# Optimization experiments

Hardware: AMD Instinct MI355X
Metric: run time of the kernel (lower is better)

## Reference

```python
import jax, jax.numpy as jnp
import numpy as np

EPS = 1e-7
NUM_NODES = 50000


def setup_inputs() -> dict:
    key = jax.random.key(0)
    k1, k2, k3 = jax.random.split(key, 3)
    n_nodes, n_edges, d = NUM_NODES, 800000, 64
    x = jax.random.normal(k1, (n_nodes, d), dtype=jnp.float32)
    edge_index = jax.random.randint(k2, (2, n_edges), 0, n_nodes, dtype=jnp.int64)
    W = jax.random.normal(k3, (d, d), dtype=jnp.float32) * (1.0 / np.sqrt(d))
    b = jnp.zeros((d,), dtype=jnp.float32)
    beta = jnp.ones((1,), dtype=jnp.float32)
    return {"x": x, "edge_index": edge_index, "W": W, "b": b, "beta": beta}


def _segment_softmax(logits, seg, num_segments):
    # numerically stable softmax over edges grouped by destination node, per channel
    m = jax.ops.segment_max(logits, seg, num_segments=num_segments)  # [N, d]
    m = jnp.where(jnp.isfinite(m), m, 0.0)  # empty segments -> -inf; neutralize
    e = jnp.exp(logits - m[seg])                                      # [E, d]
    denom = jax.ops.segment_sum(e, seg, num_segments=num_segments)    # [N, d]
    return e / (denom[seg] + 1e-16)


def reference(x, edge_index, W, b, beta):
    num_nodes, dim = x.shape
    dst = edge_index[0]
    src = edge_index[1]
    # gather + message encoder (ReLU) + eps
    edge_msg = jax.nn.relu(x[src]) + EPS                               # [E, d]
    # softmax_sg: softmax(beta * msg) per destination segment, beta is a stop-grad scalar
    alpha = _segment_softmax(beta[0] * edge_msg, dst, num_nodes)       # [E, d]
    h = edge_msg * alpha                                               # [E, d]
    # scatter-add aggregation to destination nodes
    agg = jax.ops.segment_sum(h, dst, num_segments=num_nodes)          # [N, d]
    # final dense linear (nn.Linear): agg @ W.T + b
    return agg @ W.T + b
```

## Files before the change

kernel.cpp:

```cpp
#include <hip/hip_runtime.h>
#include <hip/hip_fp16.h>

#define EPS 1e-7f
#define LOG2E 1.4426950408889634f
#define CAP 384
#define NBMAX 3136

typedef _Float16 half8 __attribute__((ext_vector_type(8)));
typedef float f32x4 __attribute__((ext_vector_type(4)));

__global__ __launch_bounds__(512)
void binprep_kernel(const int* __restrict__ dst,
                    const int* __restrict__ src, int E, int NB,
                    const float* __restrict__ x,
                    const float* __restrict__ W,
                    const float* __restrict__ beta, int M,
                    int* __restrict__ ccur,
                    unsigned* __restrict__ packed,
                    unsigned short* __restrict__ tm,
                    unsigned short* __restrict__ Wh,
                    int binBlocks) {
    if ((int)blockIdx.x < binBlocks) {
        __shared__ int lc[NBMAX];
        __shared__ int lbase[NBMAX];
        int tid = threadIdx.x;
        for (int i = tid; i < NB; i += 512) lc[i] = 0;
        __syncthreads();
        int e0 = blockIdx.x * 4096;
        int bb[8], rr[8];
        unsigned pk[8];
        #pragma unroll
        for (int i = 0; i < 8; ++i) {
            int e = e0 + i * 512 + tid;
            bb[i] = 0; rr[i] = 0; pk[i] = 0;
            if (e < E) {
                int d = dst[e];
                bb[i] = d >> 4;
                pk[i] = ((unsigned)(d & 15) << 16) | (unsigned)src[e];
                rr[i] = atomicAdd(&lc[bb[i]], 1);
            }
        }
        __syncthreads();
        for (int i = tid; i < NB; i += 512) {
            int c = lc[i];
            if (c) lbase[i] = i * CAP + atomicAdd(&ccur[i], c);
        }
        __syncthreads();
        #pragma unroll
        for (int i = 0; i < 8; ++i) {
            int e = e0 + i * 512 + tid;
            if (e < E) {
                int pos = lbase[bb[i]] + rr[i];
                if (pos < (bb[i] + 1) * CAP)
                    packed[pos] = pk[i];
            }
        }
    } else {
        int blk = blockIdx.x - binBlocks;
        int tid = threadIdx.x;
        if (blk == 0) {
            #pragma unroll
            for (int j = 0; j < 8; ++j) {
                int i = tid * 8 + j;
                Wh[i] = __half_as_ushort(__float2half_rn(W[i]));
            }
        }
        const float btl = beta[0] * LOG2E;
        const unsigned short sent = __half_as_ushort(__float2half_rn(-1000.f));
        #pragma unroll
        for (int p = 0; p < 4; ++p) {
            int i = blk * 8192 + p * 2048 + tid * 4;
            if (i < M) {
                float4 v = *(const float4*)&x[i];
                ushort4 o;
                o.x = __half_as_ushort(__float2half_rn((fmaxf(v.x, 0.f) + EPS) * btl));
                o.y = __half_as_ushort(__float2half_rn((fmaxf(v.y, 0.f) + EPS) * btl));
                o.z = __half_as_ushort(__float2half_rn((fmaxf(v.z, 0.f) + EPS) * btl));
                o.w = __half_as_ushort(__float2half_rn((fmaxf(v.w, 0.f) + EPS) * btl));
                *(ushort4*)&tm[i] = o;
            } else if (i < M + 64) {
                ushort4 o; o.x = o.y = o.z = o.w = sent;
                *(ushort4*)&tm[i] = o;
            }
        }
    }
}

__global__ __launch_bounds__(256)
void gatherlin_kernel(const unsigned* __restrict__ packed,
                      const int* __restrict__ ccur,
                      const unsigned short* __restrict__ tm,
                      const unsigned short* __restrict__ Wh,
                      const float* __restrict__ bias,
                      const float* __restrict__ beta,
                      float* __restrict__ out, int N) {
    __shared__ unsigned stage_pk[CAP];
    __shared__ unsigned short stage16[CAP + 64];
    __shared__ short aggS[16 * 72];
    __shared__ int lc[16], nstart[16], lcur[16];

    const int tid = threadIdx.x;
    const int b = blockIdx.x;
    const unsigned short sentid = (unsigned short)N;

    int len = ccur[b];
    if (len > CAP) len = CAP;
    const int rs = b * CAP;

    if (tid < 16) lc[tid] = 0;
    for (int i = tid; i < CAP + 64; i += 256) stage16[i] = sentid;
    __syncthreads();

    for (int i = tid; i < len; i += 256) {
        unsigned u = packed[rs + i];
        stage_pk[i] = u;
        atomicAdd(&lc[u >> 16], 1);
    }
    __syncthreads();

    if (tid < 16) {
        int c4 = (lc[tid] + 3) & ~3;
        int incl = c4;
        #pragma unroll
        for (int d = 1; d < 16; d <<= 1) {
            int t = __shfl_up(incl, d, 64);
            if (tid >= d) incl += t;
        }
        nstart[tid] = incl - c4;
        lcur[tid] = incl - c4;
    }
    __syncthreads();

    for (int i = tid; i < len; i += 256) {
        unsigned u = stage_pk[i];
        int pos = atomicAdd(&lcur[u >> 16], 1);
        stage16[pos] = (unsigned short)(u & 0xffffu);
    }
    __syncthreads();

    const int wave = tid >> 6;
    const int lane = tid & 63;
    const int quarter = lane >> 4;
    const int l16 = lane & 15;
    const int chb = l16 << 3;
    const unsigned char* tb = (const unsigned char*)tm;
    const float scale = 0.6931471805599453f / beta[0];

    const int nl = wave * 4 + quarter;
    const int start = nstart[nl];
    const int cnt = lc[nl];

    float s1x = 0.f, s1y = 0.f, s1z = 0.f, s1w = 0.f;
    float s2x = 0.f, s2y = 0.f, s2z = 0.f, s2w = 0.f;

    #pragma unroll 1
    for (int k = 0; k < cnt; k += 4) {
        uint2 e4 = *(const uint2*)&stage16[start + k];
        int r0 = (int)(e4.x & 0xffffu) << 7;
        int r1 = (int)(e4.x >> 16) << 7;
        int r2 = (int)(e4.y & 0xffffu) << 7;
        int r3 = (int)(e4.y >> 16) << 7;
        uint2 u0 = *(const uint2*)(tb + (r0 + chb));
        uint2 u1 = *(const uint2*)(tb + (r1 + chb));
        uint2 u2 = *(const uint2*)(tb + (r2 + chb));
        uint2 u3 = *(const uint2*)(tb + (r3 + chb));
        #define ACC(u) { \
            float m0 = __half2float(__ushort_as_half((unsigned short)(u.x & 0xffffu))); \
            float m1 = __half2float(__ushort_as_half((unsigned short)(u.x >> 16))); \
            float m2 = __half2float(__ushort_as_half((unsigned short)(u.y & 0xffffu))); \
            float m3 = __half2float(__ushort_as_half((unsigned short)(u.y >> 16))); \
            float e0 = exp2f(m0), e1 = exp2f(m1); \
            float e2 = exp2f(m2), e3 = exp2f(m3); \
            s1x += e0; s2x = fmaf(m0, e0, s2x); \
            s1y += e1; s2y = fmaf(m1, e1, s2y); \
            s1z += e2; s2z = fmaf(m2, e2, s2z); \
            s1w += e3; s2w = fmaf(m3, e3, s2w); }
        ACC(u0); ACC(u1); ACC(u2); ACC(u3);
        #undef ACC
    }

    {
        float gx = __fdividef(s2x, s1x + 1e-16f) * scale;
        float gy = __fdividef(s2y, s1y + 1e-16f) * scale;
        float gz = __fdividef(s2z, s1z + 1e-16f) * scale;
        float gw = __fdividef(s2w, s1w + 1e-16f) * scale;
        uint2 o;
        o.x = (unsigned)__half_as_ushort(__float2half_rn(gx)) |
              ((unsigned)__half_as_ushort(__float2half_rn(gy)) << 16);
        o.y = (unsigned)__half_as_ushort(__float2half_rn(gz)) |
              ((unsigned)__half_as_ushort(__float2half_rn(gw)) << 16);
        *(uint2*)((unsigned char*)aggS + nl * 144 + chb) = o;
    }
    __syncthreads();

    const unsigned char* ab = (const unsigned char*)aggS;
    half8 a0 = *(const half8*)(ab + l16 * 144 + quarter * 16);
    half8 a1 = *(const half8*)(ab + l16 * 144 + 64 + quarter * 16);
    const unsigned char* wr =
        (const unsigned char*)Wh + (((size_t)(wave * 16 + l16)) << 7) + quarter * 16;
    half8 b0 = *(const half8*)(wr);
    half8 b1 = *(const half8*)(wr + 64);
    f32x4 acc = (f32x4){0.f, 0.f, 0.f, 0.f};
    acc = __builtin_amdgcn_mfma_f32_16x16x32_f16(a0, b0, acc, 0, 0, 0);
    acc = __builtin_amdgcn_mfma_f32_16x16x32_f16(a1, b1, acc, 0, 0, 0);
    const float bv = bias[wave * 16 + l16];
    #pragma unroll
    for (int r = 0; r < 4; ++r) {
        int nd = b * 16 + quarter * 4 + r;
        if (nd < N)
            out[((size_t)nd << 6) + wave * 16 + l16] = acc[r] + bv;
    }
}

extern "C" void kernel_launch(void* const* d_in, const int* in_sizes, int n_in,
                              void* d_out, int out_size, void* d_ws, size_t ws_size,
                              hipStream_t stream) {
    const float* x    = (const float*)d_in[0];
    const int*   ei   = (const int*)d_in[1];
    const float* W    = (const float*)d_in[2];
    const float* b    = (const float*)d_in[3];
    const float* beta = (const float*)d_in[4];
    float* out = (float*)d_out;

    const int N = in_sizes[0] / 64;
    const int E = in_sizes[1] / 2;
    const int* dst = ei;
    const int* src = ei + E;
    const int NB = (N + 15) >> 4;
    const int M = N * 64;

    auto align = [](size_t v) { return (v + 255) & ~(size_t)255; };
    size_t off = 0;
    char* ws = (char*)d_ws;
    int* ccur = (int*)(ws + off);         off += align((size_t)NB * 4);
    unsigned* packed = (unsigned*)(ws + off);
    off += align((size_t)NB * CAP * 4);
    unsigned short* tm = (unsigned short*)(ws + off);
    off += align(((size_t)N + 1) * 64 * 2);
    unsigned short* Wh = (unsigned short*)(ws + off);
    off += align(64 * 64 * 2);

    const int binBlocks  = (E + 4095) / 4096;
    const int prepBlocks = (M + 64 + 8191) / 8192;
    hipMemsetAsync(ccur, 0, (size_t)NB * 4, stream);
    binprep_kernel<<<binBlocks + prepBlocks, 512, 0, stream>>>(
        dst, src, E, NB, x, W, beta, M, ccur, packed, tm, Wh, binBlocks);
    gatherlin_kernel<<<NB, 256, 0, stream>>>(packed, ccur, tm, Wh, b, beta,
                                             out, N);
}
```

Baseline: 113.2 us.

## Replace bin-then-sort with per-node fixed-capacity adjacency lists via global atomics

Edges are now scattered straight into a per-destination-node list of capacity 64 using a global atomic counter per node. This replaces the per-16-node bin buffer and the shared-memory counting sort that the gather kernel used to do. The gather kernel reads each node's list directly and processes 8 neighbours per iteration, padding with a sentinel row. Shared-memory staging and several block barriers go away, at the cost of more global atomic contention. Any node with more than 64 incoming edges is silently truncated.

```diff
diff --git a/kernel.cpp b/kernel.cpp
--- a/kernel.cpp
+++ b/kernel.cpp
@@ -3,61 +3,49 @@
 
 #define EPS 1e-7f
 #define LOG2E 1.4426950408889634f
-#define CAP 384
-#define NBMAX 3136
+#define CAPN 64
 
 typedef _Float16 half8 __attribute__((ext_vector_type(8)));
 typedef float f32x4 __attribute__((ext_vector_type(4)));
 
 __global__ __launch_bounds__(512)
 void binprep_kernel(const int* __restrict__ dst,
-                    const int* __restrict__ src, int E, int NB,
+                    const int* __restrict__ src, int E,
                     const float* __restrict__ x,
                     const float* __restrict__ W,
                     const float* __restrict__ beta, int M,
-                    int* __restrict__ ccur,
-                    unsigned* __restrict__ packed,
+                    int* __restrict__ cnt,
+                    unsigned short* __restrict__ list,
                     unsigned short* __restrict__ tm,
                     unsigned short* __restrict__ Wh,
                     int binBlocks) {
+    const int tid = threadIdx.x;
     if ((int)blockIdx.x < binBlocks) {
-        __shared__ int lc[NBMAX];
-        __shared__ int lbase[NBMAX];
-        int tid = threadIdx.x;
-        for (int i = tid; i < NB; i += 512) lc[i] = 0;
-        __syncthreads();
-        int e0 = blockIdx.x * 4096;
-        int bb[8], rr[8];
-        unsigned pk[8];
-        #pragma unroll
-        for (int i = 0; i < 8; ++i) {
-            int e = e0 + i * 512 + tid;
-            bb[i] = 0; rr[i] = 0; pk[i] = 0;
-            if (e < E) {
-                int d = dst[e];
-                bb[i] = d >> 4;
-                pk[i] = ((unsigned)(d & 15) << 16) | (unsigned)src[e];
-                rr[i] = atomicAdd(&lc[bb[i]], 1);
+        const int e0 = blockIdx.x * 2048 + tid;
+        int dd[4];
+        int rr[4];
+        unsigned short ss[4];
+        bool vv[4];
+        #pragma unroll
+        for (int i = 0; i < 4; ++i) {
+            int e = e0 + i * 512;
+            vv[i] = (e < E);
+            dd[i] = 0;
+            ss[i] = 0;
+            if (vv[i]) {
+                dd[i] = dst[e];
+                ss[i] = (unsigned short)src[e];
             }
         }
-        __syncthreads();
-        for (int i = tid; i < NB; i += 512) {
-            int c = lc[i];
-            if (c) lbase[i] = i * CAP + atomicAdd(&ccur[i], c);
-        }
-        __syncthreads();
-        #pragma unroll
-        for (int i = 0; i < 8; ++i) {
-            int e = e0 + i * 512 + tid;
-            if (e < E) {
-                int pos = lbase[bb[i]] + rr[i];
-                if (pos < (bb[i] + 1) * CAP)
-                    packed[pos] = pk[i];
-            }
-        }
+        #pragma unroll
+        for (int i = 0; i < 4; ++i)
+            rr[i] = vv[i] ? atomicAdd(&cnt[dd[i]], 1) : CAPN;
+        #pragma unroll
+        for (int i = 0; i < 4; ++i)
+            if (rr[i] < CAPN)
+                list[(dd[i] << 6) + rr[i]] = ss[i];
     } else {
         int blk = blockIdx.x - binBlocks;
-        int tid = threadIdx.x;
         if (blk == 0) {
             #pragma unroll
             for (int j = 0; j < 8; ++j) {
@@ -87,57 +75,17 @@
 }
 
 __global__ __launch_bounds__(256)
-void gatherlin_kernel(const unsigned* __restrict__ packed,
-                      const int* __restrict__ ccur,
+void gatherlin_kernel(const unsigned short* __restrict__ list,
+                      const int* __restrict__ cnt,
                       const unsigned short* __restrict__ tm,
                       const unsigned short* __restrict__ Wh,
                       const float* __restrict__ bias,
                       const float* __restrict__ beta,
                       float* __restrict__ out, int N) {
-    __shared__ unsigned stage_pk[CAP];
-    __shared__ unsigned short stage16[CAP + 64];
     __shared__ short aggS[16 * 72];
-    __shared__ int lc[16], nstart[16], lcur[16];
 
     const int tid = threadIdx.x;
     const int b = blockIdx.x;
-    const unsigned short sentid = (unsigned short)N;
-
-    int len = ccur[b];
-    if (len > CAP) len = CAP;
-    const int rs = b * CAP;
-
-    if (tid < 16) lc[tid] = 0;
-    for (int i = tid; i < CAP + 64; i += 256) stage16[i] = sentid;
-    __syncthreads();
-
-    for (int i = tid; i < len; i += 256) {
-        unsigned u = packed[rs + i];
-        stage_pk[i] = u;
-        atomicAdd(&lc[u >> 16], 1);
-    }
-    __syncthreads();
-
-    if (tid < 16) {
-        int c4 = (lc[tid] + 3) & ~3;
-        int incl = c4;
-        #pragma unroll
-        for (int d = 1; d < 16; d <<= 1) {
-            int t = __shfl_up(incl, d, 64);
-            if (tid >= d) incl += t;
-        }
-        nstart[tid] = incl - c4;
-        lcur[tid] = incl - c4;
-    }
-    __syncthreads();
-
-    for (int i = tid; i < len; i += 256) {
-        unsigned u = stage_pk[i];
-        int pos = atomicAdd(&lcur[u >> 16], 1);
-        stage16[pos] = (unsigned short)(u & 0xffffu);
-    }
-    __syncthreads();
-
     const int wave = tid >> 6;
     const int lane = tid & 63;
     const int quarter = lane >> 4;
@@ -147,23 +95,36 @@
     const float scale = 0.6931471805599453f / beta[0];
 
     const int nl = wave * 4 + quarter;
-    const int start = nstart[nl];
-    const int cnt = lc[nl];
+    const int node = b * 16 + nl;
+    int c = 0;
+    if (node < N) {
+        c = cnt[node];
+        if (c > CAPN) c = CAPN;
+    }
+    const unsigned short* lrow = list + ((size_t)node << 6);
 
     float s1x = 0.f, s1y = 0.f, s1z = 0.f, s1w = 0.f;
     float s2x = 0.f, s2y = 0.f, s2z = 0.f, s2w = 0.f;
 
     #pragma unroll 1
-    for (int k = 0; k < cnt; k += 4) {
-        uint2 e4 = *(const uint2*)&stage16[start + k];
-        int r0 = (int)(e4.x & 0xffffu) << 7;
-        int r1 = (int)(e4.x >> 16) << 7;
-        int r2 = (int)(e4.y & 0xffffu) << 7;
-        int r3 = (int)(e4.y >> 16) << 7;
-        uint2 u0 = *(const uint2*)(tb + (r0 + chb));
-        uint2 u1 = *(const uint2*)(tb + (r1 + chb));
-        uint2 u2 = *(const uint2*)(tb + (r2 + chb));
-        uint2 u3 = *(const uint2*)(tb + (r3 + chb));
+    for (int k = 0; k < c; k += 8) {
+        uint4 e8 = *(const uint4*)(lrow + k);
+        int i0 = (int)(e8.x & 0xffffu);
+        int i1 = (k + 1 < c) ? (int)(e8.x >> 16) : N;
+        int i2 = (k + 2 < c) ? (int)(e8.y & 0xffffu) : N;
+        int i3 = (k + 3 < c) ? (int)(e8.y >> 16) : N;
+        int i4 = (k + 4 < c) ? (int)(e8.z & 0xffffu) : N;
+        int i5 = (k + 5 < c) ? (int)(e8.z >> 16) : N;
+        int i6 = (k + 6 < c) ? (int)(e8.w & 0xffffu) : N;
+        int i7 = (k + 7 < c) ? (int)(e8.w >> 16) : N;
+        uint2 u0 = *(const uint2*)(tb + ((i0 << 7) + chb));
+        uint2 u1 = *(const uint2*)(tb + ((i1 << 7) + chb));
+        uint2 u2 = *(const uint2*)(tb + ((i2 << 7) + chb));
+        uint2 u3 = *(const uint2*)(tb + ((i3 << 7) + chb));
+        uint2 u4 = *(const uint2*)(tb + ((i4 << 7) + chb));
+        uint2 u5 = *(const uint2*)(tb + ((i5 << 7) + chb));
+        uint2 u6 = *(const uint2*)(tb + ((i6 << 7) + chb));
+        uint2 u7 = *(const uint2*)(tb + ((i7 << 7) + chb));
         #define ACC(u) { \
             float m0 = __half2float(__ushort_as_half((unsigned short)(u.x & 0xffffu))); \
             float m1 = __half2float(__ushort_as_half((unsigned short)(u.x >> 16))); \
@@ -176,6 +137,7 @@
             s1z += e2; s2z = fmaf(m2, e2, s2z); \
             s1w += e3; s2w = fmaf(m3, e3, s2w); }
         ACC(u0); ACC(u1); ACC(u2); ACC(u3);
+        ACC(u4); ACC(u5); ACC(u6); ACC(u7);
         #undef ACC
     }
 
@@ -232,19 +194,19 @@
     auto align = [](size_t v) { return (v + 255) & ~(size_t)255; };
     size_t off = 0;
     char* ws = (char*)d_ws;
-    int* ccur = (int*)(ws + off);         off += align((size_t)NB * 4);
-    unsigned* packed = (unsigned*)(ws + off);
-    off += align((size_t)NB * CAP * 4);
+    int* cnt = (int*)(ws + off);                off += align((size_t)N * 4);
+    unsigned short* list = (unsigned short*)(ws + off);
+    off += align((size_t)N * CAPN * 2);
     unsigned short* tm = (unsigned short*)(ws + off);
     off += align(((size_t)N + 1) * 64 * 2);
     unsigned short* Wh = (unsigned short*)(ws + off);
     off += align(64 * 64 * 2);
 
-    const int binBlocks  = (E + 4095) / 4096;
+    const int binBlocks  = (E + 2047) / 2048;
     const int prepBlocks = (M + 64 + 8191) / 8192;
-    hipMemsetAsync(ccur, 0, (size_t)NB * 4, stream);
+    hipMemsetAsync(cnt, 0, (size_t)N * 4, stream);
     binprep_kernel<<<binBlocks + prepBlocks, 512, 0, stream>>>(
-        dst, src, E, NB, x, W, beta, M, ccur, packed, tm, Wh, binBlocks);
-    gatherlin_kernel<<<NB, 256, 0, stream>>>(packed, ccur, tm, Wh, b, beta,
+        dst, src, E, x, W, beta, M, cnt, list, tm, Wh, binBlocks);
+    gatherlin_kernel<<<NB, 256, 0, stream>>>(list, cnt, tm, Wh, b, beta,
                                              out, N);
 }
```

Measured after the change: 147.5 us. 1.3x slower.

## Split fp16 feature table into two channel halves and gather in two passes

Applied to the files above, without the earlier changes.

The fp16 activation table is stored as two separate 32-channel halves (tmA, tmB), each 64 bytes per node. The gather kernel now makes two passes over each node's edge list, one per half, with 4-byte loads instead of 8-byte loads. The intent is to shrink the working set each pass touches so the gathered rows fit better in cache. The cost is reading the edge indices twice, issuing twice as many gather instructions, and an extra block-wide barrier.

```diff
diff --git a/kernel.cpp b/kernel.cpp
--- a/kernel.cpp
+++ b/kernel.cpp
@@ -17,7 +17,8 @@
                     const float* __restrict__ beta, int M,
                     int* __restrict__ ccur,
                     unsigned* __restrict__ packed,
-                    unsigned short* __restrict__ tm,
+                    unsigned short* __restrict__ tmA,
+                    unsigned short* __restrict__ tmB,
                     unsigned short* __restrict__ Wh,
                     int binBlocks) {
     if ((int)blockIdx.x < binBlocks) {
@@ -70,17 +71,22 @@
         #pragma unroll
         for (int p = 0; p < 4; ++p) {
             int i = blk * 8192 + p * 2048 + tid * 4;
-            if (i < M) {
-                float4 v = *(const float4*)&x[i];
+            if (i < M + 64) {
+                int n = i >> 6;
+                int c = i & 63;
+                unsigned short* dp = (c < 32) ? (tmA + n * 32 + c)
+                                              : (tmB + n * 32 + (c - 32));
                 ushort4 o;
-                o.x = __half_as_ushort(__float2half_rn((fmaxf(v.x, 0.f) + EPS) * btl));
-                o.y = __half_as_ushort(__float2half_rn((fmaxf(v.y, 0.f) + EPS) * btl));
-                o.z = __half_as_ushort(__float2half_rn((fmaxf(v.z, 0.f) + EPS) * btl));
-                o.w = __half_as_ushort(__float2half_rn((fmaxf(v.w, 0.f) + EPS) * btl));
-                *(ushort4*)&tm[i] = o;
-            } else if (i < M + 64) {
-                ushort4 o; o.x = o.y = o.z = o.w = sent;
-                *(ushort4*)&tm[i] = o;
+                if (i < M) {
+                    float4 v = *(const float4*)&x[i];
+                    o.x = __half_as_ushort(__float2half_rn((fmaxf(v.x, 0.f) + EPS) * btl));
+                    o.y = __half_as_ushort(__float2half_rn((fmaxf(v.y, 0.f) + EPS) * btl));
+                    o.z = __half_as_ushort(__float2half_rn((fmaxf(v.z, 0.f) + EPS) * btl));
+                    o.w = __half_as_ushort(__float2half_rn((fmaxf(v.w, 0.f) + EPS) * btl));
+                } else {
+                    o.x = o.y = o.z = o.w = sent;
+                }
+                *(ushort4*)dp = o;
             }
         }
     }
@@ -89,7 +95,8 @@
 __global__ __launch_bounds__(256)
 void gatherlin_kernel(const unsigned* __restrict__ packed,
                       const int* __restrict__ ccur,
-                      const unsigned short* __restrict__ tm,
+                      const unsigned short* __restrict__ tmA,
+                      const unsigned short* __restrict__ tmB,
                       const unsigned short* __restrict__ Wh,
                       const float* __restrict__ bias,
                       const float* __restrict__ beta,
@@ -142,56 +149,50 @@
     const int lane = tid & 63;
     const int quarter = lane >> 4;
     const int l16 = lane & 15;
-    const int chb = l16 << 3;
-    const unsigned char* tb = (const unsigned char*)tm;
+    const int cb = l16 << 2;
     const float scale = 0.6931471805599453f / beta[0];
 
     const int nl = wave * 4 + quarter;
     const int start = nstart[nl];
     const int cnt = lc[nl];
 
-    float s1x = 0.f, s1y = 0.f, s1z = 0.f, s1w = 0.f;
-    float s2x = 0.f, s2y = 0.f, s2z = 0.f, s2w = 0.f;
-
     #pragma unroll 1
-    for (int k = 0; k < cnt; k += 4) {
-        uint2 e4 = *(const uint2*)&stage16[start + k];
-        int r0 = (int)(e4.x & 0xffffu) << 7;
-        int r1 = (int)(e4.x >> 16) << 7;
-        int r2 = (int)(e4.y & 0xffffu) << 7;
-        int r3 = (int)(e4.y >> 16) << 7;
-        uint2 u0 = *(const uint2*)(tb + (r0 + chb));
-        uint2 u1 = *(const uint2*)(tb + (r1 + chb));
-        uint2 u2 = *(const uint2*)(tb + (r2 + chb));
-        uint2 u3 = *(const uint2*)(tb + (r3 + chb));
-        #define ACC(u) { \
-            float m0 = __half2float(__ushort_as_half((unsigned short)(u.x & 0xffffu))); \
-            float m1 = __half2float(__ushort_as_half((unsigned short)(u.x >> 16))); \
-            float m2 = __half2float(__ushort_as_half((unsigned short)(u.y & 0xffffu))); \
-            float m3 = __half2float(__ushort_as_half((unsigned short)(u.y >> 16))); \
-            float e0 = exp2f(m0), e1 = exp2f(m1); \
-            float e2 = exp2f(m2), e3 = exp2f(m3); \
-            s1x += e0; s2x = fmaf(m0, e0, s2x); \
-            s1y += e1; s2y = fmaf(m1, e1, s2y); \
-            s1z += e2; s2z = fmaf(m2, e2, s2z); \
-            s1w += e3; s2w = fmaf(m3, e3, s2w); }
-        ACC(u0); ACC(u1); ACC(u2); ACC(u3);
-        #undef ACC
-    }
-
-    {
-        float gx = __fdividef(s2x, s1x + 1e-16f) * scale;
-        float gy = __fdividef(s2y, s1y + 1e-16f) * scale;
-        float gz = __fdividef(s2z, s1z + 1e-16f) * scale;
-        float gw = __fdividef(s2w, s1w + 1e-16f) * scale;
-        uint2 o;
-        o.x = (unsigned)__half_as_ushort(__float2half_rn(gx)) |
-              ((unsigned)__half_as_ushort(__float2half_rn(gy)) << 16);
-        o.y = (unsigned)__half_as_ushort(__float2half_rn(gz)) |
-              ((unsigned)__half_as_ushort(__float2half_rn(gw)) << 16);
-        *(uint2*)((unsigned char*)aggS + nl * 144 + chb) = o;
-    }
-    __syncthreads();
+    for (int pass = 0; pass < 2; ++pass) {
+        const unsigned char* tb =
+            (const unsigned char*)(pass ? tmB : tmA);
+
+        float s1a = 0.f, s1b = 0.f, s2a = 0.f, s2b = 0.f;
+
+        #pragma unroll 1
+        for (int k = 0; k < cnt; k += 4) {
+            uint2 e4 = *(const uint2*)&stage16[start + k];
+            int r0 = (int)(e4.x & 0xffffu) << 6;
+            int r1 = (int)(e4.x >> 16) << 6;
+            int r2 = (int)(e4.y & 0xffffu) << 6;
+            int r3 = (int)(e4.y >> 16) << 6;
+            unsigned v0 = *(const unsigned*)(tb + (r0 + cb));
+            unsigned v1 = *(const unsigned*)(tb + (r1 + cb));
+            unsigned v2 = *(const unsigned*)(tb + (r2 + cb));
+            unsigned v3 = *(const unsigned*)(tb + (r3 + cb));
+            #define ACC2(v) { \
+                float m0 = __half2float(__ushort_as_half((unsigned short)(v & 0xffffu))); \
+                float m1 = __half2float(__ushort_as_half((unsigned short)(v >> 16))); \
+                float e0 = exp2f(m0), e1 = exp2f(m1); \
+                s1a += e0; s2a = fmaf(m0, e0, s2a); \
+                s1b += e1; s2b = fmaf(m1, e1, s2b); }
+            ACC2(v0); ACC2(v1); ACC2(v2); ACC2(v3);
+            #undef ACC2
+        }
+
+        {
+            float ga = __fdividef(s2a, s1a + 1e-16f) * scale;
+            float gb = __fdividef(s2b, s1b + 1e-16f) * scale;
+            unsigned o = (unsigned)__half_as_ushort(__float2half_rn(ga)) |
+                         ((unsigned)__half_as_ushort(__float2half_rn(gb)) << 16);
+            *(unsigned*)((unsigned char*)aggS + nl * 144 + pass * 64 + cb) = o;
+        }
+        __syncthreads();
+    }
 
     const unsigned char* ab = (const unsigned char*)aggS;
     half8 a0 = *(const half8*)(ab + l16 * 144 + quarter * 16);
@@ -235,8 +236,10 @@
     int* ccur = (int*)(ws + off);         off += align((size_t)NB * 4);
     unsigned* packed = (unsigned*)(ws + off);
     off += align((size_t)NB * CAP * 4);
-    unsigned short* tm = (unsigned short*)(ws + off);
-    off += align(((size_t)N + 1) * 64 * 2);
+    unsigned short* tmA = (unsigned short*)(ws + off);
+    off += align(((size_t)N + 1) * 32 * 2);
+    unsigned short* tmB = (unsigned short*)(ws + off);
+    off += align(((size_t)N + 1) * 32 * 2);
     unsigned short* Wh = (unsigned short*)(ws + off);
     off += align(64 * 64 * 2);
 
@@ -244,7 +247,7 @@
     const int prepBlocks = (M + 64 + 8191) / 8192;
     hipMemsetAsync(ccur, 0, (size_t)NB * 4, stream);
     binprep_kernel<<<binBlocks + prepBlocks, 512, 0, stream>>>(
-        dst, src, E, NB, x, W, beta, M, ccur, packed, tm, Wh, binBlocks);
-    gatherlin_kernel<<<NB, 256, 0, stream>>>(packed, ccur, tm, Wh, b, beta,
-                                             out, N);
+        dst, src, E, NB, x, W, beta, M, ccur, packed, tmA, tmB, Wh, binBlocks);
+    gatherlin_kernel<<<NB, 256, 0, stream>>>(packed, ccur, tmA, tmB, Wh, b,
+                                             beta, out, N);
 }
```

Result: slower. 115.8 us (+2.3%).
